# Kernel optimization log

Hardware: AMD Instinct MI355X
Metric: run time of the kernel (lower is better)

Reference implementation:

```python
import jax, jax.numpy as jnp
import numpy as np

D_MODEL, NHEAD = 1024, 16
DK = D_MODEL // NHEAD


def setup_inputs() -> dict:
    key = jax.random.key(0)
    ks = jax.random.split(key, 10)
    B, T = 2, 2048
    s = 1.0 / np.sqrt(D_MODEL)
    inp = {
        "x": jax.random.normal(ks[0], (B, T, D_MODEL), dtype=jnp.float32),
        "attn_bias": jax.random.normal(ks[1], (1, NHEAD, T, T), dtype=jnp.float32),
        "Wq": jax.random.normal(ks[2], (D_MODEL, D_MODEL), dtype=jnp.float32) * s,
        "bq": jnp.zeros((D_MODEL,), dtype=jnp.float32),
        "Wk": jax.random.normal(ks[3], (D_MODEL, D_MODEL), dtype=jnp.float32) * s,
        "bk": jnp.zeros((D_MODEL,), dtype=jnp.float32),
        "Wv": jax.random.normal(ks[4], (D_MODEL, D_MODEL), dtype=jnp.float32) * s,
        "bv": jnp.zeros((D_MODEL,), dtype=jnp.float32),
        "Wo": jax.random.normal(ks[5], (D_MODEL, D_MODEL), dtype=jnp.float32) * s,
        "bo": jnp.zeros((D_MODEL,), dtype=jnp.float32),
    }
    return inp


def reference(x, attn_bias, Wq, bq, Wk, bk, Wv, bv, Wo, bo):
    B, T, D = x.shape
    H, dk = NHEAD, DK
    # torch Linear: y = x @ W.T + b
    q = (x @ Wq.T + bq).reshape(B, T, H, dk).transpose(0, 2, 1, 3)  # [B,H,T,dk]
    k = (x @ Wk.T + bk).reshape(B, T, H, dk).transpose(0, 2, 1, 3)
    v = (x @ Wv.T + bv).reshape(B, T, H, dk).transpose(0, 2, 1, 3)
    scores = jnp.einsum("bhqd,bhkd->bhqk", q, k) / jnp.sqrt(jnp.float32(dk))
    scores = scores + attn_bias  # broadcast over batch
    attn = jax.nn.softmax(scores, axis=-1)  # dropout p=0.0 -> identity
    out = jnp.einsum("bhqk,bhkd->bhqd", attn, v)
    out = out.transpose(0, 2, 1, 3).reshape(B, T, D)
    return out @ Wo.T + bo
```

## Files before the change

### kernel.cpp

```cpp
#include <hip/hip_runtime.h>

typedef unsigned short u16;
typedef unsigned int u32;
using short8 = __attribute__((ext_vector_type(8))) short;
using f32x4  = __attribute__((ext_vector_type(4))) float;

#define D_MODEL 1024
#define NHEAD 16
#define DKV 64
#define TSEQ 2048
#define BATCH 2
#define L2E 1.44269504f
#define CSHIFT 12.0f

__device__ __forceinline__ u16 f2bf(float f) {
    union { float f; u32 i; } c; c.f = f;
    u32 x = c.i;
    return (u16)((x + 0x7FFFu + ((x >> 16) & 1u)) >> 16);
}
__device__ __forceinline__ u16 f2bf_fast(float f) {
    union { float f; u32 i; } c; c.f = f;
    return (u16)((c.i + 0x8000u) >> 16);
}

__global__ __launch_bounds__(256) void prep_cvt(
    const float* __restrict__ x,  const float* __restrict__ Wq,
    const float* __restrict__ Wk, const float* __restrict__ Wv,
    const float* __restrict__ Wo, u16* __restrict__ dst)
{
    size_t e = ((size_t)blockIdx.x * 256 + threadIdx.x) * 8;
    const float* src; size_t off;
    if (e < 4194304u)      { src = x;  off = e; }
    else if (e < 5242880u) { src = Wq; off = e - 4194304u; }
    else if (e < 6291456u) { src = Wk; off = e - 5242880u; }
    else if (e < 7340032u) { src = Wv; off = e - 6291456u; }
    else                   { src = Wo; off = e - 7340032u; }
    float4 a = *(const float4*)(src + off);
    float4 b = *(const float4*)(src + off + 4);
    short8 v;
    v[0] = (short)f2bf(a.x); v[1] = (short)f2bf(a.y);
    v[2] = (short)f2bf(a.z); v[3] = (short)f2bf(a.w);
    v[4] = (short)f2bf(b.x); v[5] = (short)f2bf(b.y);
    v[6] = (short)f2bf(b.z); v[7] = (short)f2bf(b.w);
    *(short8*)(dst + e) = v;
}

__global__ __launch_bounds__(256) void qkv_gemm(
    const u16* __restrict__ xbf, const u16* __restrict__ wbf,
    const float* __restrict__ bq, const float* __restrict__ bk,
    const float* __restrict__ bv, u16* __restrict__ qkv)
{
    __shared__ __align__(16) u16 Alds[128 * 72];
    __shared__ __align__(16) u16 Blds[128 * 72];

    const int fid = blockIdx.x;
    const int xcd = fid & 7, ii = fid >> 3;
    const int z = ii >> 5, r2 = ii & 31;
    const int nb = r2 & 7, mb = xcd * 4 + (r2 >> 3);
    const int n0 = nb * 128, m0 = mb * 128;
    const u16* W = wbf + (size_t)z * 1048576;
    const float* bias = (z == 0) ? bq : (z == 1) ? bk : bv;
    u16* out = qkv + (size_t)z * 4194304;

    const int t = threadIdx.x;
    const int wave = t >> 6, lane = t & 63, l15 = lane & 15, quad = lane >> 4;
    const int wm = (wave >> 1) * 64, wn = (wave & 1) * 64;

    f32x4 acc[4][4];
#pragma unroll
    for (int i = 0; i < 4; ++i)
#pragma unroll
        for (int j = 0; j < 4; ++j)
#pragma unroll
            for (int r = 0; r < 4; ++r) acc[i][j][r] = 0.f;

    const int srow = t >> 3, sc8 = (t & 7) * 8;

    for (int kt = 0; kt < 16; ++kt) {
        const int k0 = kt * 64;
#pragma unroll
        for (int p = 0; p < 4; ++p) {
            int row = p * 32 + srow;
            *(short8*)&Alds[row * 72 + sc8] =
                *(const short8*)&xbf[(size_t)(m0 + row) * 1024 + k0 + sc8];
            *(short8*)&Blds[row * 72 + sc8] =
                *(const short8*)&W[(size_t)(n0 + row) * 1024 + k0 + sc8];
        }
        __syncthreads();
#pragma unroll
        for (int ki = 0; ki < 2; ++ki) {
            short8 af[4], bfr[4];
#pragma unroll
            for (int i = 0; i < 4; ++i)
                af[i] = *(const short8*)&Alds[(wm + i * 16 + l15) * 72 + ki * 32 + quad * 8];
#pragma unroll
            for (int j = 0; j < 4; ++j)
                bfr[j] = *(const short8*)&Blds[(wn + j * 16 + l15) * 72 + ki * 32 + quad * 8];
#pragma unroll
            for (int i = 0; i < 4; ++i)
#pragma unroll
                for (int j = 0; j < 4; ++j)
                    acc[i][j] = __builtin_amdgcn_mfma_f32_16x16x32_bf16(af[i], bfr[j], acc[i][j], 0, 0, 0);
        }
        __syncthreads();
    }

#pragma unroll
    for (int j = 0; j < 4; ++j) {
        int n = n0 + wn + j * 16 + l15;
        float bb = bias[n];
        int h = n >> 6, d = n & 63;
#pragma unroll
        for (int i = 0; i < 4; ++i)
#pragma unroll
            for (int r = 0; r < 4; ++r) {
                int m = m0 + wm + i * 16 + quad * 4 + r;
                int bidx = m >> 11, tt = m & 2047;
                out[(((size_t)(bidx * NHEAD + h)) * TSEQ + tt) * DKV + d] =
                    f2bf(acc[i][j][r] + bb);
            }
    }
}

__global__ __launch_bounds__(256) void attn_kernel(
    const u16* __restrict__ qws, const u16* __restrict__ kws, const u16* __restrict__ vws,
    const float* __restrict__ bias, u16* __restrict__ ows)
{
    __shared__ __align__(16) u16 Klds[64 * 72];
    __shared__ __align__(16) u16 Vt[2][64 * 72];
    __shared__ __align__(16) u16 Plds[64 * 72];

    const int fid = blockIdx.x;
    const int xcd = fid & 7, ii = fid >> 3;
    const int bh = xcd * 4 + (ii >> 5);
    const int qt = ii & 31;
    const int h = bh & 15;
    const int q0 = qt * 64;
    const int t = threadIdx.x;
    const int wave = t >> 6, lane = t & 63, l15 = lane & 15, quad = lane >> 4;
    const size_t bhoff = (size_t)bh * TSEQ * DKV;

    short8 qa0, qa1;
    {
        const u16* qp = qws + bhoff + (size_t)(q0 + wave * 16 + l15) * DKV;
        qa0 = *(const short8*)(qp + quad * 8);
        qa1 = *(const short8*)(qp + 32 + quad * 8);
    }

    float l_run[4] = {0.f, 0.f, 0.f, 0.f};
    f32x4 o_acc[4];
#pragma unroll
    for (int db = 0; db < 4; ++db)
#pragma unroll
        for (int r = 0; r < 4; ++r) o_acc[db][r] = 0.f;

    const float* bias_h = bias + ((size_t)h * TSEQ + q0) * TSEQ;
    const int a8 = t & 7, c8 = a8 * 8, rp = t >> 3;
    const int rbase = wave * 16 + quad * 4;

    for (int kt = 0; kt < TSEQ / 64; ++kt) {
        const int kc0 = kt * 64;
        u16* vtb = &Vt[kt & 1][0];

        float bz[16];
#pragma unroll
        for (int cb = 0; cb < 4; ++cb)
#pragma unroll
            for (int r = 0; r < 4; ++r)
                bz[cb * 4 + r] =
                    bias_h[(size_t)(rbase + r) * TSEQ + kc0 + cb * 16 + l15];

        {
            const u16* kp = kws + bhoff + (size_t)(kc0 + rp) * DKV + c8;
            short8 k0 = *(const short8*)kp;
            short8 k1 = *(const short8*)(kp + 32 * DKV);
            *(short8*)&Klds[rp * 72 + c8] = k0;
            *(short8*)&Klds[(rp + 32) * 72 + c8] = k1;
        }
        {
            const u16* vp = vws + bhoff + (size_t)(kc0 + 2 * rp) * DKV + c8;
            short8 v0 = *(const short8*)vp;
            short8 v1 = *(const short8*)(vp + DKV);
            int bk = rp >> 2;
            int kcl = (2 * rp) & 7;
#pragma unroll
            for (int j = 0; j < 8; ++j) {
                int d = c8 + j;
                u32 val = ((u32)(u16)v0[j]) | (((u32)(u16)v1[j]) << 16);
                *(u32*)&vtb[d * 72 + ((bk ^ a8) * 8) + kcl] = val;
            }
        }
        __syncthreads();

        f32x4 s[4];
#pragma unroll
        for (int cb = 0; cb < 4; ++cb)
#pragma unroll
            for (int r = 0; r < 4; ++r) s[cb][r] = 0.f;
#pragma unroll
        for (int cb = 0; cb < 4; ++cb) {
            const u16* kr = &Klds[(cb * 16 + l15) * 72 + quad * 8];
            short8 kb0 = *(const short8*)kr;
            short8 kb1 = *(const short8*)(kr + 32);
            s[cb] = __builtin_amdgcn_mfma_f32_16x16x32_bf16(qa0, kb0, s[cb], 0, 0, 0);
            s[cb] = __builtin_amdgcn_mfma_f32_16x16x32_bf16(qa1, kb1, s[cb], 0, 0, 0);
        }

#pragma unroll
        for (int cb = 0; cb < 4; ++cb)
#pragma unroll
            for (int r = 0; r < 4; ++r) {
                float arg = fmaf(s[cb][r], 0.125f * L2E,
                                 fmaf(bz[cb * 4 + r], L2E, -CSHIFT * L2E));
                float p = exp2f(fminf(arg, 43.f));
                l_run[r] += p;
                Plds[(rbase + r) * 72 + cb * 16 + l15] = f2bf_fast(p);
            }
        __syncthreads();

        {
            const u16* pr = &Plds[(wave * 16 + l15) * 72 + quad * 8];
            short8 pa0 = *(const short8*)pr;
            short8 pa1 = *(const short8*)(pr + 32);
#pragma unroll
            for (int db = 0; db < 4; ++db) {
                int d = db * 16 + l15;
                int sw = (d >> 3) & 7;
                const u16* vr = &vtb[d * 72];
                short8 vb0 = *(const short8*)(vr + ((quad ^ sw) * 8));
                short8 vb1 = *(const short8*)(vr + (((4 + quad) ^ sw) * 8));
                o_acc[db] = __builtin_amdgcn_mfma_f32_16x16x32_bf16(pa0, vb0, o_acc[db], 0, 0, 0);
                o_acc[db] = __builtin_amdgcn_mfma_f32_16x16x32_bf16(pa1, vb1, o_acc[db], 0, 0, 0);
            }
        }
    }

#pragma unroll
    for (int r = 0; r < 4; ++r) {
        float v = l_run[r];
        v += __shfl_xor(v, 1);
        v += __shfl_xor(v, 2);
        v += __shfl_xor(v, 4);
        v += __shfl_xor(v, 8);
        l_run[r] = v;
    }
#pragma unroll
    for (int r = 0; r < 4; ++r) {
        float inv = 1.f / l_run[r];
        int row = q0 + rbase + r;
#pragma unroll
        for (int db = 0; db < 4; ++db)
            ows[bhoff + (size_t)row * DKV + db * 16 + l15] = f2bf(o_acc[db][r] * inv);
    }
}

__global__ __launch_bounds__(256) void out_gemm(
    const u16* __restrict__ ows, const u16* __restrict__ wobf,
    const float* __restrict__ bo, float* __restrict__ out)
{
    __shared__ __align__(16) u16 Alds[128 * 72];
    __shared__ __align__(16) u16 Blds[128 * 72];

    const int fid = blockIdx.x;
    const int xcd = fid & 7, ii = fid >> 3;
    const int nb = ii & 7, mb = xcd * 4 + (ii >> 3);
    const int n0 = nb * 128, m0 = mb * 128;

    const int t = threadIdx.x;
    const int wave = t >> 6, lane = t & 63, l15 = lane & 15, quad = lane >> 4;
    const int wm = (wave >> 1) * 64, wn = (wave & 1) * 64;

    f32x4 acc[4][4];
#pragma unroll
    for (int i = 0; i < 4; ++i)
#pragma unroll
        for (int j = 0; j < 4; ++j)
#pragma unroll
            for (int r = 0; r < 4; ++r) acc[i][j][r] = 0.f;

    const int srow = t >> 3, sc8 = (t & 7) * 8;

    for (int kt = 0; kt < 16; ++kt) {
        const int k0 = kt * 64;
#pragma unroll
        for (int p = 0; p < 4; ++p) {
            int row = p * 32 + srow;
            int m = m0 + row;
            int bidx = m >> 11, tt = m & 2047;
            *(short8*)&Alds[row * 72 + sc8] =
                *(const short8*)&ows[(((size_t)(bidx * NHEAD + kt)) * TSEQ + tt) * DKV + sc8];
            *(short8*)&Blds[row * 72 + sc8] =
                *(const short8*)&wobf[(size_t)(n0 + row) * 1024 + k0 + sc8];
        }
        __syncthreads();
#pragma unroll
        for (int ki = 0; ki < 2; ++ki) {
            short8 af[4], bfr[4];
#pragma unroll
            for (int i = 0; i < 4; ++i)
                af[i] = *(const short8*)&Alds[(wm + i * 16 + l15) * 72 + ki * 32 + quad * 8];
#pragma unroll
            for (int j = 0; j < 4; ++j)
                bfr[j] = *(const short8*)&Blds[(wn + j * 16 + l15) * 72 + ki * 32 + quad * 8];
#pragma unroll
            for (int i = 0; i < 4; ++i)
#pragma unroll
                for (int j = 0; j < 4; ++j)
                    acc[i][j] = __builtin_amdgcn_mfma_f32_16x16x32_bf16(af[i], bfr[j], acc[i][j], 0, 0, 0);
        }
        __syncthreads();
    }

#pragma unroll
    for (int j = 0; j < 4; ++j) {
        int n = n0 + wn + j * 16 + l15;
        float bb = bo[n];
#pragma unroll
        for (int i = 0; i < 4; ++i)
#pragma unroll
            for (int r = 0; r < 4; ++r) {
                int m = m0 + wm + i * 16 + quad * 4 + r;
                out[(size_t)m * 1024 + n] = acc[i][j][r] + bb;
            }
    }
}

extern "C" void kernel_launch(void* const* d_in, const int* in_sizes, int n_in,
                              void* d_out, int out_size, void* d_ws, size_t ws_size,
                              hipStream_t stream)
{
    const float* x  = (const float*)d_in[0];
    const float* ab = (const float*)d_in[1];
    const float* Wq = (const float*)d_in[2];
    const float* bq = (const float*)d_in[3];
    const float* Wk = (const float*)d_in[4];
    const float* bk = (const float*)d_in[5];
    const float* Wv = (const float*)d_in[6];
    const float* bv = (const float*)d_in[7];
    const float* Wo = (const float*)d_in[8];
    const float* bo = (const float*)d_in[9];
    float* out = (float*)d_out;

    u16* wsu = (u16*)d_ws;
    const size_t WBF = 4194304;
    const size_t QKV = 8388608;
    const size_t OWS = 20971520;
    const size_t QSZ = 4194304;

    prep_cvt<<<4096, 256, 0, stream>>>(x, Wq, Wk, Wv, Wo, wsu);
    qkv_gemm<<<768, 256, 0, stream>>>(wsu, wsu + WBF, bq, bk, bv, wsu + QKV);
    attn_kernel<<<1024, 256, 0, stream>>>(wsu + QKV, wsu + QKV + QSZ,
                                          wsu + QKV + 2 * QSZ, ab, wsu + OWS);
    out_gemm<<<256, 256, 0, stream>>>(wsu + OWS, wsu + WBF + 3 * 1048576, bo, out);
}
```

Before: 505.9 us.

## Use direct global-to-LDS loads, pre-transpose V in QKV GEMM, remap attention blocks

Replaces the register-staged global→LDS tile copies in all three GEMM/attention kernels with global_load_lds 16-byte direct transfers into unpadded 64-wide LDS tiles. The QKV GEMM now writes V already transposed ([b,h,d,t]), so the attention kernel loads V^T straight into LDS instead of transposing it with scattered 32-bit stores. Attention block mapping is changed so the two batches sharing a head sit on the same XCD, aiming for L2 reuse of the attention bias. Dropping the 72-element padding may bring LDS bank conflicts on the MFMA fragment reads, and the transposed V stores are narrower (8-byte) strided writes.

```diff
diff --git a/kernel.cpp b/kernel.cpp
--- a/kernel.cpp
+++ b/kernel.cpp
@@ -4,6 +4,7 @@
 typedef unsigned int u32;
 using short8 = __attribute__((ext_vector_type(8))) short;
 using f32x4  = __attribute__((ext_vector_type(4))) float;
+using u16x4  = __attribute__((ext_vector_type(4))) u16;
 
 #define D_MODEL 1024
 #define NHEAD 16
@@ -21,6 +22,11 @@
 __device__ __forceinline__ u16 f2bf_fast(float f) {
     union { float f; u32 i; } c; c.f = f;
     return (u16)((c.i + 0x8000u) >> 16);
+}
+__device__ __forceinline__ void gl_lds16(const u16* g, u16* l) {
+    __builtin_amdgcn_global_load_lds(
+        (const __attribute__((address_space(1))) void*)g,
+        (__attribute__((address_space(3))) void*)l, 16, 0, 0);
 }
 
 __global__ __launch_bounds__(256) void prep_cvt(
@@ -48,10 +54,11 @@
 __global__ __launch_bounds__(256) void qkv_gemm(
     const u16* __restrict__ xbf, const u16* __restrict__ wbf,
     const float* __restrict__ bq, const float* __restrict__ bk,
-    const float* __restrict__ bv, u16* __restrict__ qkv)
-{
-    __shared__ __align__(16) u16 Alds[128 * 72];
-    __shared__ __align__(16) u16 Blds[128 * 72];
+    const float* __restrict__ bv,
+    u16* __restrict__ qws, u16* __restrict__ kws, u16* __restrict__ vtws)
+{
+    __shared__ __align__(16) u16 Alds[128 * 64];
+    __shared__ __align__(16) u16 Blds[128 * 64];
 
     const int fid = blockIdx.x;
     const int xcd = fid & 7, ii = fid >> 3;
@@ -59,12 +66,11 @@
     const int nb = r2 & 7, mb = xcd * 4 + (r2 >> 3);
     const int n0 = nb * 128, m0 = mb * 128;
     const u16* W = wbf + (size_t)z * 1048576;
-    const float* bias = (z == 0) ? bq : (z == 1) ? bk : bv;
-    u16* out = qkv + (size_t)z * 4194304;
 
     const int t = threadIdx.x;
     const int wave = t >> 6, lane = t & 63, l15 = lane & 15, quad = lane >> 4;
     const int wm = (wave >> 1) * 64, wn = (wave & 1) * 64;
+    const int lrow = lane >> 3, lcol = (lane & 7) * 8;
 
     f32x4 acc[4][4];
 #pragma unroll
@@ -73,18 +79,16 @@
         for (int j = 0; j < 4; ++j)
 #pragma unroll
             for (int r = 0; r < 4; ++r) acc[i][j][r] = 0.f;
-
-    const int srow = t >> 3, sc8 = (t & 7) * 8;
 
     for (int kt = 0; kt < 16; ++kt) {
         const int k0 = kt * 64;
 #pragma unroll
-        for (int p = 0; p < 4; ++p) {
-            int row = p * 32 + srow;
-            *(short8*)&Alds[row * 72 + sc8] =
-                *(const short8*)&xbf[(size_t)(m0 + row) * 1024 + k0 + sc8];
-            *(short8*)&Blds[row * 72 + sc8] =
-                *(const short8*)&W[(size_t)(n0 + row) * 1024 + k0 + sc8];
+        for (int ra = 0; ra < 4; ++ra) {
+            int row0 = ra * 32 + wave * 8;
+            gl_lds16(&xbf[(size_t)(m0 + row0 + lrow) * 1024 + k0 + lcol],
+                     &Alds[row0 * 64 + lane * 8]);
+            gl_lds16(&W[(size_t)(n0 + row0 + lrow) * 1024 + k0 + lcol],
+                     &Blds[row0 * 64 + lane * 8]);
         }
         __syncthreads();
 #pragma unroll
@@ -92,10 +96,10 @@
             short8 af[4], bfr[4];
 #pragma unroll
             for (int i = 0; i < 4; ++i)
-                af[i] = *(const short8*)&Alds[(wm + i * 16 + l15) * 72 + ki * 32 + quad * 8];
+                af[i] = *(const short8*)&Alds[(wm + i * 16 + l15) * 64 + ki * 32 + quad * 8];
 #pragma unroll
             for (int j = 0; j < 4; ++j)
-                bfr[j] = *(const short8*)&Blds[(wn + j * 16 + l15) * 72 + ki * 32 + quad * 8];
+                bfr[j] = *(const short8*)&Blds[(wn + j * 16 + l15) * 64 + ki * 32 + quad * 8];
 #pragma unroll
             for (int i = 0; i < 4; ++i)
 #pragma unroll
@@ -105,36 +109,57 @@
         __syncthreads();
     }
 
-#pragma unroll
-    for (int j = 0; j < 4; ++j) {
-        int n = n0 + wn + j * 16 + l15;
-        float bb = bias[n];
-        int h = n >> 6, d = n & 63;
-#pragma unroll
-        for (int i = 0; i < 4; ++i)
-#pragma unroll
-            for (int r = 0; r < 4; ++r) {
-                int m = m0 + wm + i * 16 + quad * 4 + r;
+    const float* bias = (z == 0) ? bq : (z == 1) ? bk : bv;
+    if (z < 2) {
+        u16* out = (z == 0) ? qws : kws;
+#pragma unroll
+        for (int j = 0; j < 4; ++j) {
+            int n = n0 + wn + j * 16 + l15;
+            float bb = bias[n];
+            int h = n >> 6, d = n & 63;
+#pragma unroll
+            for (int i = 0; i < 4; ++i)
+#pragma unroll
+                for (int r = 0; r < 4; ++r) {
+                    int m = m0 + wm + i * 16 + quad * 4 + r;
+                    int bidx = m >> 11, tt = m & 2047;
+                    out[(((size_t)(bidx * NHEAD + h)) * TSEQ + tt) * DKV + d] =
+                        f2bf(acc[i][j][r] + bb);
+                }
+        }
+    } else {
+#pragma unroll
+        for (int j = 0; j < 4; ++j) {
+            int n = n0 + wn + j * 16 + l15;
+            float bb = bias[n];
+            int h = n >> 6, d = n & 63;
+#pragma unroll
+            for (int i = 0; i < 4; ++i) {
+                int m = m0 + wm + i * 16 + quad * 4;
                 int bidx = m >> 11, tt = m & 2047;
-                out[(((size_t)(bidx * NHEAD + h)) * TSEQ + tt) * DKV + d] =
-                    f2bf(acc[i][j][r] + bb);
+                u16x4 pv;
+#pragma unroll
+                for (int r = 0; r < 4; ++r) pv[r] = f2bf(acc[i][j][r] + bb);
+                *(u16x4*)&vtws[((size_t)(bidx * NHEAD + h) * DKV + d) * TSEQ + tt] = pv;
             }
+        }
     }
 }
 
 __global__ __launch_bounds__(256) void attn_kernel(
-    const u16* __restrict__ qws, const u16* __restrict__ kws, const u16* __restrict__ vws,
-    const float* __restrict__ bias, u16* __restrict__ ows)
-{
-    __shared__ __align__(16) u16 Klds[64 * 72];
-    __shared__ __align__(16) u16 Vt[2][64 * 72];
+    const u16* __restrict__ qws, const u16* __restrict__ kws,
+    const u16* __restrict__ vtws, const float* __restrict__ bias,
+    u16* __restrict__ ows)
+{
+    __shared__ __align__(16) u16 Klds[64 * 64];
+    __shared__ __align__(16) u16 Vt[2][64 * 64];
     __shared__ __align__(16) u16 Plds[64 * 72];
 
     const int fid = blockIdx.x;
     const int xcd = fid & 7, ii = fid >> 3;
-    const int bh = xcd * 4 + (ii >> 5);
-    const int qt = ii & 31;
-    const int h = bh & 15;
+    const int b = ii & 1, j = ii >> 1;
+    const int qt = j & 31, h = xcd * 2 + (j >> 5);
+    const int bh = b * NHEAD + h;
     const int q0 = qt * 64;
     const int t = threadIdx.x;
     const int wave = t >> 6, lane = t & 63, l15 = lane & 15, quad = lane >> 4;
@@ -155,13 +180,21 @@
         for (int r = 0; r < 4; ++r) o_acc[db][r] = 0.f;
 
     const float* bias_h = bias + ((size_t)h * TSEQ + q0) * TSEQ;
-    const int a8 = t & 7, c8 = a8 * 8, rp = t >> 3;
+    const int lrow = lane >> 3, lcol = (lane & 7) * 8;
     const int rbase = wave * 16 + quad * 4;
 
     for (int kt = 0; kt < TSEQ / 64; ++kt) {
         const int kc0 = kt * 64;
         u16* vtb = &Vt[kt & 1][0];
 
+#pragma unroll
+        for (int rr = 0; rr < 2; ++rr) {
+            int row0 = rr * 32 + wave * 8;
+            gl_lds16(&kws[bhoff + (size_t)(kc0 + row0 + lrow) * DKV + lcol],
+                     &Klds[row0 * 64 + lane * 8]);
+            gl_lds16(&vtws[bhoff + (size_t)(row0 + lrow) * TSEQ + kc0 + lcol],
+                     &vtb[row0 * 64 + lane * 8]);
+        }
         float bz[16];
 #pragma unroll
         for (int cb = 0; cb < 4; ++cb)
@@ -169,27 +202,6 @@
             for (int r = 0; r < 4; ++r)
                 bz[cb * 4 + r] =
                     bias_h[(size_t)(rbase + r) * TSEQ + kc0 + cb * 16 + l15];
-
-        {
-            const u16* kp = kws + bhoff + (size_t)(kc0 + rp) * DKV + c8;
-            short8 k0 = *(const short8*)kp;
-            short8 k1 = *(const short8*)(kp + 32 * DKV);
-            *(short8*)&Klds[rp * 72 + c8] = k0;
-            *(short8*)&Klds[(rp + 32) * 72 + c8] = k1;
-        }
-        {
-            const u16* vp = vws + bhoff + (size_t)(kc0 + 2 * rp) * DKV + c8;
-            short8 v0 = *(const short8*)vp;
-            short8 v1 = *(const short8*)(vp + DKV);
-            int bk = rp >> 2;
-            int kcl = (2 * rp) & 7;
-#pragma unroll
-            for (int j = 0; j < 8; ++j) {
-                int d = c8 + j;
-                u32 val = ((u32)(u16)v0[j]) | (((u32)(u16)v1[j]) << 16);
-                *(u32*)&vtb[d * 72 + ((bk ^ a8) * 8) + kcl] = val;
-            }
-        }
         __syncthreads();
 
         f32x4 s[4];
@@ -199,7 +211,7 @@
             for (int r = 0; r < 4; ++r) s[cb][r] = 0.f;
 #pragma unroll
         for (int cb = 0; cb < 4; ++cb) {
-            const u16* kr = &Klds[(cb * 16 + l15) * 72 + quad * 8];
+            const u16* kr = &Klds[(cb * 16 + l15) * 64 + quad * 8];
             short8 kb0 = *(const short8*)kr;
             short8 kb1 = *(const short8*)(kr + 32);
             s[cb] = __builtin_amdgcn_mfma_f32_16x16x32_bf16(qa0, kb0, s[cb], 0, 0, 0);
@@ -224,11 +236,9 @@
             short8 pa1 = *(const short8*)(pr + 32);
 #pragma unroll
             for (int db = 0; db < 4; ++db) {
-                int d = db * 16 + l15;
-                int sw = (d >> 3) & 7;
-                const u16* vr = &vtb[d * 72];
-                short8 vb0 = *(const short8*)(vr + ((quad ^ sw) * 8));
-                short8 vb1 = *(const short8*)(vr + (((4 + quad) ^ sw) * 8));
+                const u16* vr = &vtb[(db * 16 + l15) * 64 + quad * 8];
+                short8 vb0 = *(const short8*)vr;
+                short8 vb1 = *(const short8*)(vr + 32);
                 o_acc[db] = __builtin_amdgcn_mfma_f32_16x16x32_bf16(pa0, vb0, o_acc[db], 0, 0, 0);
                 o_acc[db] = __builtin_amdgcn_mfma_f32_16x16x32_bf16(pa1, vb1, o_acc[db], 0, 0, 0);
             }
@@ -258,8 +268,8 @@
     const u16* __restrict__ ows, const u16* __restrict__ wobf,
     const float* __restrict__ bo, float* __restrict__ out)
 {
-    __shared__ __align__(16) u16 Alds[128 * 72];
-    __shared__ __align__(16) u16 Blds[128 * 72];
+    __shared__ __align__(16) u16 Alds[128 * 64];
+    __shared__ __align__(16) u16 Blds[128 * 64];
 
     const int fid = blockIdx.x;
     const int xcd = fid & 7, ii = fid >> 3;
@@ -269,6 +279,7 @@
     const int t = threadIdx.x;
     const int wave = t >> 6, lane = t & 63, l15 = lane & 15, quad = lane >> 4;
     const int wm = (wave >> 1) * 64, wn = (wave & 1) * 64;
+    const int lrow = lane >> 3, lcol = (lane & 7) * 8;
 
     f32x4 acc[4][4];
 #pragma unroll
@@ -277,20 +288,18 @@
         for (int j = 0; j < 4; ++j)
 #pragma unroll
             for (int r = 0; r < 4; ++r) acc[i][j][r] = 0.f;
-
-    const int srow = t >> 3, sc8 = (t & 7) * 8;
 
     for (int kt = 0; kt < 16; ++kt) {
         const int k0 = kt * 64;
 #pragma unroll
-        for (int p = 0; p < 4; ++p) {
-            int row = p * 32 + srow;
-            int m = m0 + row;
+        for (int ra = 0; ra < 4; ++ra) {
+            int row0 = ra * 32 + wave * 8;
+            int m = m0 + row0 + lrow;
             int bidx = m >> 11, tt = m & 2047;
-            *(short8*)&Alds[row * 72 + sc8] =
-                *(const short8*)&ows[(((size_t)(bidx * NHEAD + kt)) * TSEQ + tt) * DKV + sc8];
-            *(short8*)&Blds[row * 72 + sc8] =
-                *(const short8*)&wobf[(size_t)(n0 + row) * 1024 + k0 + sc8];
+            gl_lds16(&ows[(((size_t)(bidx * NHEAD + kt)) * TSEQ + tt) * DKV + lcol],
+                     &Alds[row0 * 64 + lane * 8]);
+            gl_lds16(&wobf[(size_t)(n0 + row0 + lrow) * 1024 + k0 + lcol],
+                     &Blds[row0 * 64 + lane * 8]);
         }
         __syncthreads();
 #pragma unroll
@@ -298,10 +307,10 @@
             short8 af[4], bfr[4];
 #pragma unroll
             for (int i = 0; i < 4; ++i)
-                af[i] = *(const short8*)&Alds[(wm + i * 16 + l15) * 72 + ki * 32 + quad * 8];
+                af[i] = *(const short8*)&Alds[(wm + i * 16 + l15) * 64 + ki * 32 + quad * 8];
 #pragma unroll
             for (int j = 0; j < 4; ++j)
-                bfr[j] = *(const short8*)&Blds[(wn + j * 16 + l15) * 72 + ki * 32 + quad * 8];
+                bfr[j] = *(const short8*)&Blds[(wn + j * 16 + l15) * 64 + ki * 32 + quad * 8];
 #pragma unroll
             for (int i = 0; i < 4; ++i)
 #pragma unroll
@@ -343,13 +352,15 @@
 
     u16* wsu = (u16*)d_ws;
     const size_t WBF = 4194304;
-    const size_t QKV = 8388608;
+    const size_t QWS = 8388608;
+    const size_t KWS = 12582912;
+    const size_t VTW = 16777216;
     const size_t OWS = 20971520;
-    const size_t QSZ = 4194304;
 
     prep_cvt<<<4096, 256, 0, stream>>>(x, Wq, Wk, Wv, Wo, wsu);
-    qkv_gemm<<<768, 256, 0, stream>>>(wsu, wsu + WBF, bq, bk, bv, wsu + QKV);
-    attn_kernel<<<1024, 256, 0, stream>>>(wsu + QKV, wsu + QKV + QSZ,
-                                          wsu + QKV + 2 * QSZ, ab, wsu + OWS);
+    qkv_gemm<<<768, 256, 0, stream>>>(wsu, wsu + WBF, bq, bk, bv,
+                                      wsu + QWS, wsu + KWS, wsu + VTW);
+    attn_kernel<<<1024, 256, 0, stream>>>(wsu + QWS, wsu + KWS, wsu + VTW,
+                                          ab, wsu + OWS);
     out_gemm<<<256, 256, 0, stream>>>(wsu + OWS, wsu + WBF + 3 * 1048576, bo, out);
 }
```

Result: slower. 519.3 us (+2.6%).
